# Performance work log

Hardware: AMD Instinct MI355X
Metric: run time of the kernel (lower is better)

Reference implementation:

```python
import jax, jax.numpy as jnp
import numpy as np

EPS = 1e-12  # matches F.normalize clamp


def sparsemax(z):
    # Martins & Astudillo sparsemax along the last axis
    K = z.shape[-1]
    z_sorted = -jnp.sort(-z, axis=-1)                      # descending
    k = jnp.arange(1, K + 1, dtype=z.dtype)
    z_cum = jnp.cumsum(z_sorted, axis=-1)
    support = (1.0 + k * z_sorted) > z_cum                 # [..., K]
    k_z = jnp.sum(support, axis=-1, keepdims=True)         # support size
    tau = (jnp.take_along_axis(z_cum, k_z - 1, axis=-1) - 1.0) / k_z.astype(z.dtype)
    return jnp.maximum(z - tau, 0.0)


def setup_inputs() -> dict:
    key = jax.random.key(0)
    k1, k2, k3 = jax.random.split(key, 3)
    B, IN, OUT = 8192, 512, 4096
    x = jax.random.normal(k1, (B, IN), dtype=jnp.float32)
    weight = jax.random.normal(k2, (OUT, IN), dtype=jnp.float32)
    lambd = jnp.square(jax.random.normal(k3, (1,), dtype=jnp.float32))  # torch init: randn**2
    return {"x": x, "weight": weight, "lambd": lambd}


def reference(x, weight, lambd):
    # normalize prototypes and inputs onto the unit hypersphere
    w_n = weight / jnp.maximum(jnp.linalg.norm(weight, axis=-1, keepdims=True), EPS)
    x_n = x / jnp.maximum(jnp.linalg.norm(x, axis=1, keepdims=True), EPS)
    xa = x_n @ w_n.T                                        # [B, OUT]
    # ||x - a||^2 via Gram expansion (avoids [B, OUT, IN] broadcast tensor)
    x2 = jnp.sum(x_n * x_n, axis=-1, keepdims=True)         # [B, 1]
    w2 = jnp.sum(w_n * w_n, axis=-1)                        # [OUT]
    sq_dist = x2 + w2[None, :] - 2.0 * xa                   # [B, OUT]
    logits = xa - lambd * sq_dist                           # kds_mode='recon_dist'
    return sparsemax(logits)
```

## Files before the change

### kernel.cpp

```cpp
#include <hip/hip_runtime.h>

typedef __attribute__((ext_vector_type(8))) short bf16x8;
typedef __attribute__((ext_vector_type(4))) float f32x4;

__device__ inline unsigned short f2bf(float f) {
  union { float f; unsigned u; } v; v.f = f;
  unsigned r = v.u + 0x7FFFu + ((v.u >> 16) & 1u);
  return (unsigned short)(r >> 16);
}

__global__ __launch_bounds__(256) void normalize_both(
    const float* __restrict__ x, const float* __restrict__ wgt,
    unsigned short* __restrict__ xb, unsigned short* __restrict__ wb) {
  const int w = threadIdx.x >> 6, lane = threadIdx.x & 63;
  const int row = blockIdx.x * 4 + w;
  const float* src;
  unsigned short* dst;
  if (row < 8192) { src = x + (size_t)row * 512;           dst = xb + (size_t)row * 512; }
  else            { src = wgt + (size_t)(row - 8192) * 512; dst = wb + (size_t)(row - 8192) * 512; }
  const float* p = src + lane * 8;
  float4 a = *reinterpret_cast<const float4*>(p);
  float4 b = *reinterpret_cast<const float4*>(p + 4);
  float ss = a.x*a.x + a.y*a.y + a.z*a.z + a.w*a.w
           + b.x*b.x + b.y*b.y + b.z*b.z + b.w*b.w;
  #pragma unroll
  for (int off = 32; off; off >>= 1) ss += __shfl_xor(ss, off);
  const float inv = 1.0f / fmaxf(sqrtf(ss), 1e-12f);
  unsigned short o[8];
  o[0]=f2bf(a.x*inv); o[1]=f2bf(a.y*inv); o[2]=f2bf(a.z*inv); o[3]=f2bf(a.w*inv);
  o[4]=f2bf(b.x*inv); o[5]=f2bf(b.y*inv); o[6]=f2bf(b.z*inv); o[7]=f2bf(b.w*inv);
  *reinterpret_cast<uint4*>(dst + lane * 8) = *reinterpret_cast<uint4*>(o);
}

#define BM 256
#define BN 256
#define BK 32

#define STAGE_A(slot_, ko_, j_)                                                   \
  do {                                                                            \
    const int c_ = wid * 2 + (j_);                                                \
    const unsigned short* s_ = Xb + (size_t)(bm0 + c_ * 16 + srow) * 512 + (ko_) + sskel; \
    __builtin_amdgcn_global_load_lds(                                             \
        (const __attribute__((address_space(1))) void*)s_,                        \
        (__attribute__((address_space(3))) void*)&As[slot_][c_ * 512], 16, 0, 0); \
  } while (0)
#define STAGE_B(slot_, ko_, j_)                                                   \
  do {                                                                            \
    const int c_ = wid * 2 + (j_);                                                \
    const unsigned short* s_ = Wb + (size_t)(bn0 + c_ * 16 + srow) * 512 + (ko_) + sskel; \
    __builtin_amdgcn_global_load_lds(                                             \
        (const __attribute__((address_space(1))) void*)s_,                        \
        (__attribute__((address_space(3))) void*)&Bs[slot_][c_ * 512], 16, 0, 0); \
  } while (0)

__global__ __launch_bounds__(512, 2) void gemm_logits_f16(
    const unsigned short* __restrict__ Xb, const unsigned short* __restrict__ Wb,
    const float* __restrict__ lambd, unsigned short* __restrict__ out16) {
  __shared__ unsigned short As[3][BM * BK];
  __shared__ unsigned short Bs[3][BN * BK];
  const int tid = threadIdx.x, lane = tid & 63, wid = tid >> 6;
  const int wm = wid >> 2, wn = wid & 3;
  const int lrow = lane & 15, kg = lane >> 4;

  const int id = (int)blockIdx.x;
  const int swz = (id & 7) * 64 + (id >> 3);
  const int bx = swz & 15;
  const int by = swz >> 4;
  const int bm0 = by * BM, bn0 = bx * BN;

  const int srow  = lane >> 2;
  const int sskel = ((lane & 3) ^ ((lane >> 3) & 3)) * 8;

  const int rswz = (lrow >> 1) & 3;
  const int kA = (kg ^ rswz) * 8;

  f32x4 acc[8][4];
  #pragma unroll
  for (int m = 0; m < 8; ++m)
    #pragma unroll
    for (int n = 0; n < 4; ++n) { f32x4 z = {0.f,0.f,0.f,0.f}; acc[m][n] = z; }

  STAGE_A(0, 0, 0); STAGE_A(0, 0, 1); STAGE_B(0, 0, 0); STAGE_B(0, 0, 1);
  STAGE_A(1, BK, 0); STAGE_A(1, BK, 1); STAGE_B(1, BK, 0); STAGE_B(1, BK, 1);
  asm volatile("s_waitcnt vmcnt(4)" ::: "memory");
  __builtin_amdgcn_s_barrier();
  __builtin_amdgcn_sched_barrier(0);

  #pragma unroll
  for (int t = 0; t < 16; ++t) {
    const int cur = t % 3, nx2 = (t + 2) % 3;
    if (t + 2 < 16) { STAGE_A(nx2, (t + 2) * BK, 0); STAGE_A(nx2, (t + 2) * BK, 1); }
    bf16x8 af0[4], bfr[4];
    #pragma unroll
    for (int mf = 0; mf < 4; ++mf)
      af0[mf] = *reinterpret_cast<const bf16x8*>(
          &As[cur][(wm * 128 + mf * 16 + lrow) * BK + kA]);
    #pragma unroll
    for (int nf = 0; nf < 4; ++nf)
      bfr[nf] = *reinterpret_cast<const bf16x8*>(
          &Bs[cur][(wn * 64 + nf * 16 + lrow) * BK + kA]);
    asm volatile("s_waitcnt lgkmcnt(0)" ::: "memory");
    __builtin_amdgcn_sched_barrier(0);
    __builtin_amdgcn_s_setprio(1);
    #pragma unroll
    for (int mf = 0; mf < 4; ++mf)
      #pragma unroll
      for (int nf = 0; nf < 4; ++nf)
        acc[mf][nf] = __builtin_amdgcn_mfma_f32_16x16x32_bf16(
            af0[mf], bfr[nf], acc[mf][nf], 0, 0, 0);
    __builtin_amdgcn_s_setprio(0);
    __builtin_amdgcn_sched_barrier(0);
    if (t + 2 < 16) { STAGE_B(nx2, (t + 2) * BK, 0); STAGE_B(nx2, (t + 2) * BK, 1); }
    bf16x8 af1[4];
    #pragma unroll
    for (int mf = 0; mf < 4; ++mf)
      af1[mf] = *reinterpret_cast<const bf16x8*>(
          &As[cur][(wm * 128 + 64 + mf * 16 + lrow) * BK + kA]);
    asm volatile("s_waitcnt lgkmcnt(0)" ::: "memory");
    __builtin_amdgcn_sched_barrier(0);
    __builtin_amdgcn_s_setprio(1);
    #pragma unroll
    for (int mf = 0; mf < 4; ++mf)
      #pragma unroll
      for (int nf = 0; nf < 4; ++nf)
        acc[mf + 4][nf] = __builtin_amdgcn_mfma_f32_16x16x32_bf16(
            af1[mf], bfr[nf], acc[mf + 4][nf], 0, 0, 0);
    __builtin_amdgcn_s_setprio(0);
    __builtin_amdgcn_sched_barrier(0);
    if (t < 15) {
      if (t < 13) { asm volatile("s_waitcnt vmcnt(4)" ::: "memory"); }
      else        { asm volatile("s_waitcnt vmcnt(0)" ::: "memory"); }
      __builtin_amdgcn_s_barrier();
      __builtin_amdgcn_sched_barrier(0);
    }
  }

  const float lam = lambd[0];
  const float sa_ = 1.0f + 2.0f * lam, sb_ = 2.0f * lam;
  #pragma unroll
  for (int mf = 0; mf < 8; ++mf) {
    #pragma unroll
    for (int nf = 0; nf < 4; ++nf) {
      const int gc = bn0 + wn * 64 + nf * 16 + lrow;
      #pragma unroll
      for (int r = 0; r < 4; ++r) {
        const int gr = bm0 + wm * 128 + mf * 16 + kg * 4 + r;
        union { _Float16 h; unsigned short u; } cv;
        cv.h = (_Float16)(sa_ * acc[mf][nf][r] - sb_);
        out16[(size_t)gr * 4096 + gc] = cv.u;
      }
    }
  }
}

__global__ __launch_bounds__(256) void sparsemax_wave(
    const unsigned short* __restrict__ zin, float* __restrict__ out) {
  const int lane = threadIdx.x & 63;
  const int row  = ((int)blockIdx.x << 2) + (threadIdx.x >> 6);
  const unsigned short* zr = zin + (size_t)row * 4096;
  float* orow = out + (size_t)row * 4096;

  float v[64];
  #pragma unroll
  for (int c = 0; c < 8; ++c) {
    uint4 pk = *reinterpret_cast<const uint4*>(&zr[c * 512 + lane * 8]);
    const unsigned short* ph = reinterpret_cast<const unsigned short*>(&pk);
    #pragma unroll
    for (int j = 0; j < 8; ++j) {
      union { unsigned short u; _Float16 h; } cv; cv.u = ph[j];
      v[c * 8 + j] = (float)cv.h;
    }
  }

  float ls = 0.f;
  #pragma unroll
  for (int j = 0; j < 64; ++j) ls += v[j];
  #pragma unroll
  for (int off = 32; off; off >>= 1) ls += __shfl_xor(ls, off);
  float tau = (ls - 1.0f) * (1.0f / 4096.0f);
  int prevC = 4096;

  for (int it = 0; it < 32; ++it) {
    float s = 0.f; int c = 0;
    #pragma unroll
    for (int j = 0; j < 64; ++j) { if (v[j] > tau) { s += v[j]; ++c; } }
    #pragma unroll
    for (int off = 32; off; off >>= 1) { s += __shfl_xor(s, off); c += __shfl_xor(c, off); }
    tau = (s - 1.0f) / (float)c;
    if (c == prevC) break;
    prevC = c;
  }

  #pragma unroll
  for (int c = 0; c < 8; ++c) {
    float4 t0, t1;
    t0.x = fmaxf(v[c*8+0] - tau, 0.f);
    t0.y = fmaxf(v[c*8+1] - tau, 0.f);
    t0.z = fmaxf(v[c*8+2] - tau, 0.f);
    t0.w = fmaxf(v[c*8+3] - tau, 0.f);
    t1.x = fmaxf(v[c*8+4] - tau, 0.f);
    t1.y = fmaxf(v[c*8+5] - tau, 0.f);
    t1.z = fmaxf(v[c*8+6] - tau, 0.f);
    t1.w = fmaxf(v[c*8+7] - tau, 0.f);
    *reinterpret_cast<float4*>(&orow[c * 512 + lane * 8])     = t0;
    *reinterpret_cast<float4*>(&orow[c * 512 + lane * 8 + 4]) = t1;
  }
}

extern "C" void kernel_launch(void* const* d_in, const int* in_sizes, int n_in,
                              void* d_out, int out_size, void* d_ws, size_t ws_size,
                              hipStream_t stream) {
  const float* x     = (const float*)d_in[0];
  const float* wgt   = (const float*)d_in[1];
  const float* lambd = (const float*)d_in[2];
  float* out = (float*)d_out;

  unsigned short* xb  = (unsigned short*)d_ws;
  unsigned short* wb  = xb + (size_t)8192 * 512;
  unsigned short* z16 = wb + (size_t)4096 * 512;

  normalize_both<<<(8192 + 4096) / 4, 256, 0, stream>>>(x, wgt, xb, wb);

  gemm_logits_f16<<<512, 512, 0, stream>>>(xb, wb, lambd, z16);

  sparsemax_wave<<<8192 / 4, 256, 0, stream>>>(z16, out);
}
```

Baseline: 95.26 us.

## Swap MFMA operands for vectorized stores and simplify GEMM main loop schedule

```diff
diff --git a/kernel.cpp b/kernel.cpp
--- a/kernel.cpp
+++ b/kernel.cpp
@@ -83,72 +83,52 @@
   STAGE_A(0, 0, 0); STAGE_A(0, 0, 1); STAGE_B(0, 0, 0); STAGE_B(0, 0, 1);
   STAGE_A(1, BK, 0); STAGE_A(1, BK, 1); STAGE_B(1, BK, 0); STAGE_B(1, BK, 1);
   asm volatile("s_waitcnt vmcnt(4)" ::: "memory");
-  __builtin_amdgcn_s_barrier();
-  __builtin_amdgcn_sched_barrier(0);
+  asm volatile("s_barrier" ::: "memory");
 
   #pragma unroll
   for (int t = 0; t < 16; ++t) {
     const int cur = t % 3, nx2 = (t + 2) % 3;
-    if (t + 2 < 16) { STAGE_A(nx2, (t + 2) * BK, 0); STAGE_A(nx2, (t + 2) * BK, 1); }
-    bf16x8 af0[4], bfr[4];
-    #pragma unroll
-    for (int mf = 0; mf < 4; ++mf)
-      af0[mf] = *reinterpret_cast<const bf16x8*>(
-          &As[cur][(wm * 128 + mf * 16 + lrow) * BK + kA]);
-    #pragma unroll
-    for (int nf = 0; nf < 4; ++nf)
-      bfr[nf] = *reinterpret_cast<const bf16x8*>(
-          &Bs[cur][(wn * 64 + nf * 16 + lrow) * BK + kA]);
-    asm volatile("s_waitcnt lgkmcnt(0)" ::: "memory");
-    __builtin_amdgcn_sched_barrier(0);
-    __builtin_amdgcn_s_setprio(1);
-    #pragma unroll
-    for (int mf = 0; mf < 4; ++mf)
+    if (t + 2 < 16) {
+      STAGE_A(nx2, (t + 2) * BK, 0); STAGE_A(nx2, (t + 2) * BK, 1);
+      STAGE_B(nx2, (t + 2) * BK, 0); STAGE_B(nx2, (t + 2) * BK, 1);
+    }
+    bf16x8 af[8], bfr[4];
+    #pragma unroll
+    for (int fr = 0; fr < 8; ++fr)
+      af[fr] = *reinterpret_cast<const bf16x8*>(
+          &As[cur][(wm * 128 + fr * 16 + lrow) * BK + kA]);
+    #pragma unroll
+    for (int fc = 0; fc < 4; ++fc)
+      bfr[fc] = *reinterpret_cast<const bf16x8*>(
+          &Bs[cur][(wn * 64 + fc * 16 + lrow) * BK + kA]);
+    #pragma unroll
+    for (int fr = 0; fr < 8; ++fr)
       #pragma unroll
-      for (int nf = 0; nf < 4; ++nf)
-        acc[mf][nf] = __builtin_amdgcn_mfma_f32_16x16x32_bf16(
-            af0[mf], bfr[nf], acc[mf][nf], 0, 0, 0);
-    __builtin_amdgcn_s_setprio(0);
-    __builtin_amdgcn_sched_barrier(0);
-    if (t + 2 < 16) { STAGE_B(nx2, (t + 2) * BK, 0); STAGE_B(nx2, (t + 2) * BK, 1); }
-    bf16x8 af1[4];
-    #pragma unroll
-    for (int mf = 0; mf < 4; ++mf)
-      af1[mf] = *reinterpret_cast<const bf16x8*>(
-          &As[cur][(wm * 128 + 64 + mf * 16 + lrow) * BK + kA]);
-    asm volatile("s_waitcnt lgkmcnt(0)" ::: "memory");
-    __builtin_amdgcn_sched_barrier(0);
-    __builtin_amdgcn_s_setprio(1);
-    #pragma unroll
-    for (int mf = 0; mf < 4; ++mf)
-      #pragma unroll
-      for (int nf = 0; nf < 4; ++nf)
-        acc[mf + 4][nf] = __builtin_amdgcn_mfma_f32_16x16x32_bf16(
-            af1[mf], bfr[nf], acc[mf + 4][nf], 0, 0, 0);
-    __builtin_amdgcn_s_setprio(0);
-    __builtin_amdgcn_sched_barrier(0);
+      for (int fc = 0; fc < 4; ++fc)
+        acc[fr][fc] = __builtin_amdgcn_mfma_f32_16x16x32_bf16(
+            bfr[fc], af[fr], acc[fr][fc], 0, 0, 0);
     if (t < 15) {
       if (t < 13) { asm volatile("s_waitcnt vmcnt(4)" ::: "memory"); }
       else        { asm volatile("s_waitcnt vmcnt(0)" ::: "memory"); }
-      __builtin_amdgcn_s_barrier();
-      __builtin_amdgcn_sched_barrier(0);
+      asm volatile("s_barrier" ::: "memory");
     }
   }
 
   const float lam = lambd[0];
   const float sa_ = 1.0f + 2.0f * lam, sb_ = 2.0f * lam;
   #pragma unroll
-  for (int mf = 0; mf < 8; ++mf) {
-    #pragma unroll
-    for (int nf = 0; nf < 4; ++nf) {
-      const int gc = bn0 + wn * 64 + nf * 16 + lrow;
-      #pragma unroll
-      for (int r = 0; r < 4; ++r) {
-        const int gr = bm0 + wm * 128 + mf * 16 + kg * 4 + r;
-        union { _Float16 h; unsigned short u; } cv;
-        cv.h = (_Float16)(sa_ * acc[mf][nf][r] - sb_);
-        out16[(size_t)gr * 4096 + gc] = cv.u;
-      }
+  for (int fr = 0; fr < 8; ++fr) {
+    const int gr = bm0 + wm * 128 + fr * 16 + lrow;
+    #pragma unroll
+    for (int fc = 0; fc < 4; ++fc) {
+      const int gc = bn0 + wn * 64 + fc * 16 + kg * 4;
+      union { _Float16 h[2]; unsigned u; } p0, p1;
+      p0.h[0] = (_Float16)(sa_ * acc[fr][fc][0] - sb_);
+      p0.h[1] = (_Float16)(sa_ * acc[fr][fc][1] - sb_);
+      p1.h[0] = (_Float16)(sa_ * acc[fr][fc][2] - sb_);
+      p1.h[1] = (_Float16)(sa_ * acc[fr][fc][3] - sb_);
+      uint2 pk; pk.x = p0.u; pk.y = p1.u;
+      *reinterpret_cast<uint2*>(&out16[(size_t)gr * 4096 + gc]) = pk;
     }
   }
 }
```

New measurement: 102.0 us. 1.07x slower.
